# Kernel tuning notes

Measured on AMD Instinct MI355X. Metric: run time of the kernel, lower is better.

Reference implementation:

```python
import jax, jax.numpy as jnp
import numpy as np

B, L, IN_DIM, D_MODEL = 4, 1024, 128, 256
MDIM = 2 * D_MODEL          # mamba_dim = 512 (must equal 2*d_model for shape consistency)
NL = 4                      # mamba_layers
DIN = 2 * MDIM              # d_inner (expand=2)
NST = 16                    # d_state
DTR = MDIM // 16            # dt_rank = 32
KC = 4                      # d_conv
EPS = 1e-5

# sinusoidal positional encoding buffer (deterministic)
_pos = np.arange(L, dtype=np.float32)[:, None]
_div = np.exp(np.arange(0, MDIM, 2, dtype=np.float32) * (-np.log(10000.0) / MDIM))
_pe = np.zeros((L, MDIM), dtype=np.float32)
_pe[:, 0::2] = np.sin(_pos * _div)
_pe[:, 1::2] = np.cos(_pos * _div)
PE = jnp.asarray(_pe)


def setup_inputs() -> dict:
    key = jax.random.key(0)
    ks = iter(jax.random.split(key, 64))
    rn = lambda shape, s=0.02: jax.random.normal(next(ks), shape, jnp.float32) * s
    inp = {
        "x": jax.random.normal(next(ks), (B, L, IN_DIM), jnp.float32),
        "rtg": jax.random.normal(next(ks), (B, L, 1), jnp.float32),
        "state_emb_w": rn((D_MODEL, IN_DIM)), "state_emb_b": jnp.zeros((D_MODEL,)),
        "reward_emb_w": rn((D_MODEL, 1)), "reward_emb_b": jnp.zeros((D_MODEL,)),
        "ln_w": jnp.ones((MDIM,)), "ln_b": jnp.zeros((MDIM,)),
        "in_proj_w": rn((NL, 2 * DIN, MDIM)),
        "conv_w": rn((NL, DIN, KC), 0.1), "conv_b": jnp.zeros((NL, DIN)),
        "x_proj_w": rn((NL, DTR + 2 * NST, DIN)),
        "dt_proj_w": rn((NL, DIN, DTR), 0.1), "dt_proj_b": jnp.full((NL, DIN), -2.0),
        "A_log": jnp.tile(jnp.log(jnp.arange(1, NST + 1, dtype=jnp.float32)), (NL, DIN, 1)),
        "D_param": jnp.ones((NL, DIN)),
        "out_proj_w": rn((NL, MDIM, DIN)),
        "norm_w": jnp.ones((NL, MDIM)), "norm_f_w": jnp.ones((MDIM,)),
        "so_w1": rn((MDIM // 2, MDIM)), "so_b1": jnp.zeros((MDIM // 2,)),
        "so_w2": rn((IN_DIM, MDIM // 2)), "so_b2": jnp.zeros((IN_DIM,)),
        "ro_w1": rn((MDIM // 2, MDIM)), "ro_b1": jnp.zeros((MDIM // 2,)),
        "ro_w2": rn((1, MDIM // 2)), "ro_b2": jnp.zeros((1,)),
    }
    return inp


def _rmsnorm(h, w):
    return h * jax.lax.rsqrt(jnp.mean(h * h, -1, keepdims=True) + EPS) * w


def _mamba(h, ipw, cw, cb, xpw, dpw, dpb, Alog, Dp, opw):
    # h: [B,L,MDIM]
    Ls = h.shape[1]
    xz = h @ ipw.T                                   # [B,L,2*DIN]
    xx, z = jnp.split(xz, 2, axis=-1)
    # causal depthwise conv, kernel KC, left pad KC-1
    xp = jnp.pad(xx, ((0, 0), (KC - 1, 0), (0, 0)))
    xc = cb + sum(cw[:, k] * xp[:, k:k + Ls, :] for k in range(KC))
    xc = jax.nn.silu(xc)                             # [B,L,DIN]
    dbc = xc @ xpw.T                                 # [B,L,DTR+2*NST]
    dt = jax.nn.softplus(dbc[..., :DTR] @ dpw.T + dpb)   # [B,L,DIN]
    Bm = dbc[..., DTR:DTR + NST]                     # [B,L,NST]
    Cm = dbc[..., DTR + NST:]                        # [B,L,NST]
    A = -jnp.exp(Alog)                               # [DIN,NST]

    def step(hc, inp):
        dt_t, B_t, C_t, x_t = inp                    # [B,DIN],[B,NST],[B,NST],[B,DIN]
        hc = jnp.exp(dt_t[:, :, None] * A) * hc + (dt_t * x_t)[:, :, None] * B_t[:, None, :]
        return hc, jnp.einsum('bdn,bn->bd', hc, C_t)

    h0 = jnp.zeros((h.shape[0], DIN, NST), h.dtype)
    _, ys = jax.lax.scan(step, h0, (dt.swapaxes(0, 1), Bm.swapaxes(0, 1),
                                    Cm.swapaxes(0, 1), xc.swapaxes(0, 1)))
    y = ys.swapaxes(0, 1) + Dp * xc
    y = y * jax.nn.silu(z)
    return y @ opw.T                                 # [B,L,MDIM]


def _forward(x, rtg, state_emb_w, state_emb_b, reward_emb_w, reward_emb_b, ln_w, ln_b,
             in_proj_w, conv_w, conv_b, x_proj_w, dt_proj_w, dt_proj_b, A_log, D_param,
             out_proj_w, norm_w, norm_f_w, so_w1, so_b1, so_w2, so_b2, ro_w1, ro_b1, ro_w2, ro_b2):
    se = x @ state_emb_w.T + state_emb_b            # [B,L,D_MODEL]
    re = rtg @ reward_emb_w.T + reward_emb_b        # [B,L,D_MODEL]
    h = jnp.concatenate([se, re], axis=-1)          # [B,L,MDIM]
    h = h + PE[:h.shape[1]]                          # dropout is identity at eval
    mu = jnp.mean(h, -1, keepdims=True)
    var = jnp.var(h, -1, keepdims=True)
    h = (h - mu) * jax.lax.rsqrt(var + EPS) * ln_w + ln_b
    residual = None
    for i in range(NL):
        residual = h if residual is None else h + residual
        hn = _rmsnorm(residual, norm_w[i])
        h = _mamba(hn, in_proj_w[i], conv_w[i], conv_b[i], x_proj_w[i],
                   dt_proj_w[i], dt_proj_b[i], A_log[i], D_param[i], out_proj_w[i])
    residual = h + residual
    h = _rmsnorm(residual, norm_f_w)
    next_state = jax.nn.relu(h @ so_w1.T + so_b1) @ so_w2.T + so_b2   # [B,L,IN_DIM]
    next_reward = jax.nn.relu(h @ ro_w1.T + ro_b1) @ ro_w2.T + ro_b2  # [B,L,1]
    return next_state, next_reward


def reference(x, rtg, state_emb_w, state_emb_b, reward_emb_w, reward_emb_b, ln_w, ln_b,
              in_proj_w, conv_w, conv_b, x_proj_w, dt_proj_w, dt_proj_b, A_log, D_param,
              out_proj_w, norm_w, norm_f_w, so_w1, so_b1, so_w2, so_b2, ro_w1, ro_b1, ro_w2, ro_b2):
    return _forward(x, rtg, state_emb_w, state_emb_b, reward_emb_w, reward_emb_b, ln_w, ln_b,
                    in_proj_w, conv_w, conv_b, x_proj_w, dt_proj_w, dt_proj_b, A_log, D_param,
                    out_proj_w, norm_w, norm_f_w, so_w1, so_b1, so_w2, so_b2, ro_w1, ro_b1, ro_w2, ro_b2)
```

## Files before the change

kernel.cpp:

```cpp
#include <hip/hip_runtime.h>
#include <stdint.h>

typedef unsigned short u16;
typedef __attribute__((ext_vector_type(8))) short bf16x8;
typedef __attribute__((ext_vector_type(8))) u16 u16x8;
typedef __attribute__((ext_vector_type(4))) float f32x4;

static __device__ __forceinline__ u16 f2b(float f) {
  uint32_t u = __builtin_bit_cast(uint32_t, f);
  u += 0x7fffu + ((u >> 16) & 1u);
  return (u16)(u >> 16);
}
static __device__ __forceinline__ float b2f(u16 h) {
  uint32_t u = ((uint32_t)h) << 16;
  return __builtin_bit_cast(float, u);
}

#define GLDS16(gsrc, ldst)                                                        \
  __builtin_amdgcn_global_load_lds(                                               \
      (const __attribute__((address_space(1))) void*)(gsrc),                      \
      (__attribute__((address_space(3))) void*)(ldst), 16, 0, 0)

__global__ __launch_bounds__(256) void setup_kernel(
    const float* __restrict__ ipw, u16* __restrict__ ipwb,
    const float* __restrict__ xpw, u16* __restrict__ xpwb,
    const float* __restrict__ opw, u16* __restrict__ opwb,
    const float* __restrict__ sow1, u16* __restrict__ sow1b,
    const float* __restrict__ sow2, u16* __restrict__ sow2b,
    const float* __restrict__ row1, u16* __restrict__ row1b,
    float* __restrict__ PEt,
    const float* __restrict__ dpw, float* __restrict__ dpwT,
    const float* __restrict__ cw, float* __restrict__ cwT,
    const float* __restrict__ Alog, float* __restrict__ A2T) {
  int i = blockIdx.x * 256 + threadIdx.x;
  if (i < 4194304) { ipwb[i] = f2b(ipw[i]); return; } i -= 4194304;
  if (i < 262144)  { xpwb[i] = f2b(xpw[i]); return; } i -= 262144;
  if (i < 2097152) { opwb[i] = f2b(opw[i]); return; } i -= 2097152;
  if (i < 131072)  { sow1b[i] = f2b(sow1[i]); return; } i -= 131072;
  if (i < 32768)   { sow2b[i] = f2b(sow2[i]); return; } i -= 32768;
  if (i < 131072)  { row1b[i] = f2b(row1[i]); return; } i -= 131072;
  if (i < 524288) {
    int dd = i & 511, l = i >> 9;
    const float cc = -9.210340371976184f / 512.f;
    float div = expf((float)(2 * (dd >> 1)) * cc);
    PEt[i] = (dd & 1) ? cosf((float)l * div) : sinf((float)l * div);
    return;
  } i -= 524288;
  if (i < 131072) {
    int l = i >> 15, r = i & 32767, j = r >> 10, dd = r & 1023;
    dpwT[i] = dpw[(size_t)l * 32768 + (size_t)dd * 32 + j];
    return;
  } i -= 131072;
  if (i < 16384) {
    int l = i >> 12, r = i & 4095, k = r >> 10, dd = r & 1023;
    cwT[i] = cw[(size_t)l * 4096 + (size_t)dd * 4 + k];
    return;
  } i -= 16384;
  if (i < 65536) {
    int l = i >> 14, r = i & 16383, n = r >> 10, d = r & 1023;
    A2T[i] = -expf(Alog[(size_t)l * 16384 + (size_t)d * 16 + n]) * 1.4426950408889634f;
  }
}

__global__ __launch_bounds__(256) void embed_ln2(
    const float* __restrict__ x, const float* __restrict__ rtg,
    const float* __restrict__ Wse, const float* __restrict__ bse,
    const float* __restrict__ Wre, const float* __restrict__ bre,
    const float* __restrict__ lnw, const float* __restrict__ lnb,
    const float* __restrict__ PEt, float* __restrict__ h) {
  const int tid = threadIdx.x;
  const int tok0 = blockIdx.x * 16;
  const int l0 = tok0 & 1023;
  __shared__ float xs[16][128];
  __shared__ float rt[16];
  __shared__ float sw[16][2][4];
  for (int i = tid; i < 16 * 128; i += 256) ((float*)xs)[i] = x[(size_t)tok0 * 128 + i];
  if (tid < 16) rt[tid] = rtg[tok0 + tid];
  __syncthreads();
  const int d = tid;
  float acc[16];
#pragma unroll
  for (int tt = 0; tt < 16; ++tt) acc[tt] = 0.f;
  const float* wrow = Wse + (size_t)d * 128;
  for (int k0 = 0; k0 < 128; k0 += 8) {
    float4 wa = *(const float4*)(wrow + k0);
    float4 wb = *(const float4*)(wrow + k0 + 4);
#pragma unroll
    for (int tt = 0; tt < 16; ++tt) {
      const float* xr = &xs[tt][k0];
      acc[tt] += xr[0] * wa.x + xr[1] * wa.y + xr[2] * wa.z + xr[3] * wa.w +
                 xr[4] * wb.x + xr[5] * wb.y + xr[6] * wb.z + xr[7] * wb.w;
    }
  }
  const float seb = bse[d], reW = Wre[d], reB = bre[d];
  const int lane = tid & 63, wv = tid >> 6;
  float h1a[16];
#pragma unroll
  for (int tt = 0; tt < 16; ++tt) {
    float h0 = acc[tt] + seb + PEt[(size_t)(l0 + tt) * 512 + d];
    float h1 = reB + rt[tt] * reW + PEt[(size_t)(l0 + tt) * 512 + 256 + d];
    acc[tt] = h0;
    h1a[tt] = h1;
    float s = h0 + h1, q = h0 * h0 + h1 * h1;
#pragma unroll
    for (int o = 32; o; o >>= 1) { s += __shfl_xor(s, o); q += __shfl_xor(q, o); }
    if (lane == 0) { sw[tt][0][wv] = s; sw[tt][1][wv] = q; }
  }
  __syncthreads();
#pragma unroll
  for (int tt = 0; tt < 16; ++tt) {
    float S = sw[tt][0][0] + sw[tt][0][1] + sw[tt][0][2] + sw[tt][0][3];
    float Q = sw[tt][1][0] + sw[tt][1][1] + sw[tt][1][2] + sw[tt][1][3];
    float mean = S * (1.f / 512.f);
    float var = Q * (1.f / 512.f) - mean * mean;
    float rstd = rsqrtf(var + 1e-5f);
    size_t base = (size_t)(tok0 + tt) * 512;
    h[base + d]       = (acc[tt] - mean) * rstd * lnw[d] + lnb[d];
    h[base + 256 + d] = (h1a[tt] - mean) * rstd * lnw[256 + d] + lnb[256 + d];
  }
}

__global__ __launch_bounds__(256) void resid_rms_kernel(
    const float* __restrict__ hin, float* __restrict__ residual,
    const float* __restrict__ w, u16* __restrict__ outb, int first) {
  const int tok = blockIdx.x;
  const int t = threadIdx.x;
  __shared__ float rq[4];
  size_t base = (size_t)tok * 512;
  float v0 = hin[base + t], v1 = hin[base + t + 256];
  if (!first) { v0 += residual[base + t]; v1 += residual[base + t + 256]; }
  residual[base + t] = v0;
  residual[base + t + 256] = v1;
  float q = v0 * v0 + v1 * v1;
#pragma unroll
  for (int o = 32; o; o >>= 1) q += __shfl_xor(q, o);
  if ((t & 63) == 0) rq[t >> 6] = q;
  __syncthreads();
  float Q = rq[0] + rq[1] + rq[2] + rq[3];
  float scale = rsqrtf(Q * (1.f / 512.f) + 1e-5f);
  outb[base + t]       = f2b(v0 * scale * w[t]);
  outb[base + t + 256] = f2b(v1 * scale * w[t + 256]);
}

template <int BM, int BN, int WM, int WN, int EPI>
__global__ __launch_bounds__(256) void gemm_bt(
    const u16* __restrict__ A, const u16* __restrict__ Bw,
    float* __restrict__ Cf, u16* __restrict__ Cb,
    const float* __restrict__ bias, const float* __restrict__ bias2,
    int M, int N, int K, int As) {
  constexpr int MF = BM / (WM * 16);
  constexpr int NF = BN / (WN * 16);
  constexpr int NCA = (BM * 4) / 256;
  constexpr int NCB = (BN * 4) / 256;
  __shared__ __align__(16) u16 lA[BM * 32];
  __shared__ __align__(16) u16 lB[BN * 32];
  const int tid = threadIdx.x;
  const int lane = tid & 63;
  const int wv = tid >> 6;
  const int wr = wv / WN, wc = wv % WN;
  const int m0 = blockIdx.x * BM, n0 = blockIdx.y * BN;
  const int kchunk = K / gridDim.z;
  const int kb = blockIdx.z * kchunk;

  f32x4 acc[MF][NF];
#pragma unroll
  for (int i = 0; i < MF; ++i)
#pragma unroll
    for (int j = 0; j < NF; ++j) acc[i][j] = (f32x4){0.f, 0.f, 0.f, 0.f};

  const int srow = tid >> 2, sck = tid & 3;
  const u16* Ag = A + (size_t)(m0 + srow) * As + sck * 8 + kb;
  const u16* Bg = Bw + (size_t)(n0 + srow) * K + sck * 8 + kb;

  for (int k0 = 0; k0 < kchunk; k0 += 32) {
#pragma unroll
    for (int it = 0; it < NCA; ++it)
      GLDS16(Ag + (size_t)it * 64 * As + k0, &lA[(it * 256 + tid) * 8]);
#pragma unroll
    for (int it = 0; it < NCB; ++it)
      GLDS16(Bg + (size_t)it * 64 * K + k0, &lB[(it * 256 + tid) * 8]);
    __syncthreads();
    bf16x8 af[MF], bfr[NF];
    const int koff = (lane >> 4) * 8;
#pragma unroll
    for (int mi = 0; mi < MF; ++mi) {
      int r = wr * (MF * 16) + mi * 16 + (lane & 15);
      af[mi] = *(const bf16x8*)(&lA[r * 32 + koff]);
    }
#pragma unroll
    for (int ni = 0; ni < NF; ++ni) {
      int r = wc * (NF * 16) + ni * 16 + (lane & 15);
      bfr[ni] = *(const bf16x8*)(&lB[r * 32 + koff]);
    }
#pragma unroll
    for (int mi = 0; mi < MF; ++mi)
#pragma unroll
      for (int ni = 0; ni < NF; ++ni)
        acc[mi][ni] = __builtin_amdgcn_mfma_f32_16x16x32_bf16(af[mi], bfr[ni], acc[mi][ni], 0, 0, 0);
    __syncthreads();
  }

  float* co = Cf + (size_t)blockIdx.z * (size_t)M * N;
  const int rbase = (lane >> 4) * 4;
  const int cbase = lane & 15;
#pragma unroll
  for (int mi = 0; mi < MF; ++mi) {
#pragma unroll
    for (int ni = 0; ni < NF; ++ni) {
      int row = m0 + wr * (MF * 16) + mi * 16 + rbase;
      int col = n0 + wc * (NF * 16) + ni * 16 + cbase;
      float bv = 0.f;
      if (EPI == 2 || EPI == 3) bv = bias[col];
      if (EPI == 4) bv = (col < 256) ? bias[col] : bias2[col - 256];
#pragma unroll
      for (int r = 0; r < 4; ++r) {
        float v = acc[mi][ni][r] + bv;
        if (EPI == 2 || EPI == 4) v = fmaxf(v, 0.f);
        size_t idx = (size_t)(row + r) * N + col;
        if (EPI == 1 || EPI == 2 || EPI == 4) Cb[idx] = f2b(v);
        else co[idx] = v;
      }
    }
  }
}

__global__ __launch_bounds__(256) void conv_silu3(
    const u16* __restrict__ xz, const float* __restrict__ cwT,
    const float* __restrict__ cb, u16* __restrict__ xcb) {
  int gid = blockIdx.x * 256 + threadIdx.x;
  int d0 = (gid & 127) * 8;
  int token = gid >> 7;
  int t = token & 1023;
  const u16* xx = xz + (size_t)(token - t) * 2048 + d0;
  float s[8];
  {
    float4 cba = *(const float4*)(cb + d0);
    float4 cbb = *(const float4*)(cb + d0 + 4);
    s[0] = cba.x; s[1] = cba.y; s[2] = cba.z; s[3] = cba.w;
    s[4] = cbb.x; s[5] = cbb.y; s[6] = cbb.z; s[7] = cbb.w;
  }
#pragma unroll
  for (int k = 0; k < 4; ++k) {
    int tt = t - 3 + k;
    if (tt >= 0) {
      u16x8 v = *(const u16x8*)(xx + (size_t)tt * 2048);
      float4 wA = *(const float4*)(cwT + (size_t)k * 1024 + d0);
      float4 wB = *(const float4*)(cwT + (size_t)k * 1024 + d0 + 4);
      s[0] += wA.x * b2f(v[0]); s[1] += wA.y * b2f(v[1]);
      s[2] += wA.z * b2f(v[2]); s[3] += wA.w * b2f(v[3]);
      s[4] += wB.x * b2f(v[4]); s[5] += wB.y * b2f(v[5]);
      s[6] += wB.z * b2f(v[6]); s[7] += wB.w * b2f(v[7]);
    }
  }
  u16x8 o;
#pragma unroll
  for (int j = 0; j < 8; ++j) {
    float sl = s[j] / (1.f + expf(-s[j]));
    o[j] = f2b(sl);
  }
  *(u16x8*)(xcb + (size_t)token * 1024 + d0) = o;
}

__global__ __launch_bounds__(256) void dt_kernel2(
    const float* __restrict__ P, const float* __restrict__ dpwT,
    const float* __restrict__ dpb, u16* __restrict__ dtout,
    float* __restrict__ dbcr) {
  const int tid = threadIdx.x;
  const int tok0 = blockIdx.x * 16;
  __shared__ float sm[16][64];
  const size_t str = (size_t)4096 * 64;
  for (int i = tid; i < 16 * 64; i += 256) {
    size_t o = (size_t)tok0 * 64 + i;
    float v = 0.f;
#pragma unroll
    for (int p = 0; p < 8; ++p) v += P[(size_t)p * str + o];
    ((float*)sm)[i] = v;
    dbcr[o] = v;
  }
  __syncthreads();
  float acc0[16], acc1[16], acc2[16], acc3[16];
#pragma unroll
  for (int t = 0; t < 16; ++t) { acc0[t] = 0.f; acc1[t] = 0.f; acc2[t] = 0.f; acc3[t] = 0.f; }
#pragma unroll 4
  for (int j = 0; j < 32; ++j) {
    float w0 = dpwT[(size_t)j * 1024 + tid];
    float w1 = dpwT[(size_t)j * 1024 + 256 + tid];
    float w2 = dpwT[(size_t)j * 1024 + 512 + tid];
    float w3 = dpwT[(size_t)j * 1024 + 768 + tid];
#pragma unroll
    for (int t = 0; t < 16; ++t) {
      float sv = sm[t][j];
      acc0[t] += sv * w0;
      acc1[t] += sv * w1;
      acc2[t] += sv * w2;
      acc3[t] += sv * w3;
    }
  }
  const float b0 = dpb[tid], b1 = dpb[256 + tid], b2 = dpb[512 + tid], b3 = dpb[768 + tid];
#pragma unroll
  for (int t = 0; t < 16; ++t) {
    size_t o = (size_t)(tok0 + t) * 1024 + tid;
    float a0 = acc0[t] + b0, a1 = acc1[t] + b1, a2 = acc2[t] + b2, a3 = acc3[t] + b3;
    dtout[o]       = f2b((a0 > 20.f) ? a0 : logf(1.f + expf(a0)));
    dtout[o + 256] = f2b((a1 > 20.f) ? a1 : logf(1.f + expf(a1)));
    dtout[o + 512] = f2b((a2 > 20.f) ? a2 : logf(1.f + expf(a2)));
    dtout[o + 768] = f2b((a3 > 20.f) ? a3 : logf(1.f + expf(a3)));
  }
}

__global__ __launch_bounds__(256) void scan1(
    const u16* __restrict__ dt, const u16* __restrict__ xc,
    const float* __restrict__ dbc, const float* __restrict__ A2T_l,
    float* __restrict__ Ubuf, float* __restrict__ SD, int NCc, int TCc) {
  const int d = blockIdx.x * 256 + threadIdx.x;
  const int c = blockIdx.y;
  const int b = blockIdx.z;
  const int t0 = c * TCc;
  __shared__ __align__(16) float sB[64][16];
  for (int i = threadIdx.x; i < TCc * 16; i += 256) {
    int t = i >> 4, n = i & 15;
    sB[t][n] = dbc[((size_t)(b * 1024 + t0 + t)) * 64 + 32 + n];
  }
  float A2[16];
#pragma unroll
  for (int n = 0; n < 16; ++n) A2[n] = A2T_l[(size_t)n * 1024 + d];
  __syncthreads();
  float hc[16];
#pragma unroll
  for (int n = 0; n < 16; ++n) hc[n] = 0.f;
  float sumdt = 0.f;
  size_t tok = (size_t)b * 1024 + t0;
  for (int t = 0; t < TCc; ++t, ++tok) {
    float dtv = b2f(dt[tok * 1024 + d]);
    float xcv = b2f(xc[tok * 1024 + d]);
    float du = dtv * xcv;
    sumdt += dtv;
#pragma unroll
    for (int q = 0; q < 4; ++q) {
      float4 B4 = *(const float4*)(&sB[t][q * 4]);
      float e0 = exp2f(dtv * A2[q * 4 + 0]);
      float e1 = exp2f(dtv * A2[q * 4 + 1]);
      float e2 = exp2f(dtv * A2[q * 4 + 2]);
      float e3 = exp2f(dtv * A2[q * 4 + 3]);
      hc[q * 4 + 0] = e0 * hc[q * 4 + 0] + du * B4.x;
      hc[q * 4 + 1] = e1 * hc[q * 4 + 1] + du * B4.y;
      hc[q * 4 + 2] = e2 * hc[q * 4 + 2] + du * B4.z;
      hc[q * 4 + 3] = e3 * hc[q * 4 + 3] + du * B4.w;
    }
  }
  size_t ob = (((size_t)b * NCc + c) * 16) * 1024 + d;
#pragma unroll
  for (int n = 0; n < 16; ++n) Ubuf[ob + (size_t)n * 1024] = hc[n];
  SD[((size_t)b * NCc + c) * 1024 + d] = sumdt;
}

__global__ __launch_bounds__(256) void scan_mid(
    const float* __restrict__ Ubuf, const float* __restrict__ SD,
    const float* __restrict__ A2T_l, float* __restrict__ H0, int NCc) {
  int idx = blockIdx.x * 256 + threadIdx.x;
  int b = idx >> 14;
  int nd = idx & 16383;
  int d = nd & 1023;
  const float A2 = A2T_l[nd];
  float h = 0.f;
  size_t o0 = ((size_t)b * NCc * 16) * 1024 + nd;
  const size_t cstr = (size_t)16 * 1024;
  size_t sd0 = ((size_t)b * NCc) * 1024 + d;
  for (int cc = 0; cc < NCc; ++cc) {
    size_t o = o0 + (size_t)cc * cstr;
    H0[o] = h;
    if (cc < NCc - 1) {
      float e = exp2f(A2 * SD[sd0 + (size_t)cc * 1024]);
      h = e * h + Ubuf[o];
    }
  }
}

__global__ __launch_bounds__(256) void scan2(
    const u16* __restrict__ dt, const u16* __restrict__ xc,
    const float* __restrict__ dbc, const u16* __restrict__ xz,
    const float* __restrict__ A2T_l, const float* __restrict__ Dp,
    const float* __restrict__ H0, u16* __restrict__ yg, int NCc, int TCc) {
  const int d = blockIdx.x * 256 + threadIdx.x;
  const int c = blockIdx.y;
  const int b = blockIdx.z;
  const int t0 = c * TCc;
  __shared__ __align__(16) float sB[64][16];
  __shared__ __align__(16) float sC[64][16];
  for (int i = threadIdx.x; i < TCc * 16; i += 256) {
    int t = i >> 4, n = i & 15;
    size_t o = ((size_t)(b * 1024 + t0 + t)) * 64 + 32;
    sB[t][n] = dbc[o + n];
    sC[t][n] = dbc[o + 16 + n];
  }
  float A2[16];
#pragma unroll
  for (int n = 0; n < 16; ++n) A2[n] = A2T_l[(size_t)n * 1024 + d];
  const float Dd = Dp[d];
  float hc[16];
  size_t ob = (((size_t)b * NCc + c) * 16) * 1024 + d;
#pragma unroll
  for (int n = 0; n < 16; ++n) hc[n] = H0[ob + (size_t)n * 1024];
  __syncthreads();
  size_t tok = (size_t)b * 1024 + t0;
  for (int t = 0; t < TCc; ++t, ++tok) {
    float dtv = b2f(dt[tok * 1024 + d]);
    float xcv = b2f(xc[tok * 1024 + d]);
    float du = dtv * xcv;
    float y0 = 0.f, y1 = 0.f, y2 = 0.f, y3 = 0.f;
#pragma unroll
    for (int q = 0; q < 4; ++q) {
      float4 B4 = *(const float4*)(&sB[t][q * 4]);
      float4 C4 = *(const float4*)(&sC[t][q * 4]);
      float e0 = exp2f(dtv * A2[q * 4 + 0]);
      float e1 = exp2f(dtv * A2[q * 4 + 1]);
      float e2 = exp2f(dtv * A2[q * 4 + 2]);
      float e3 = exp2f(dtv * A2[q * 4 + 3]);
      hc[q * 4 + 0] = e0 * hc[q * 4 + 0] + du * B4.x;
      hc[q * 4 + 1] = e1 * hc[q * 4 + 1] + du * B4.y;
      hc[q * 4 + 2] = e2 * hc[q * 4 + 2] + du * B4.z;
      hc[q * 4 + 3] = e3 * hc[q * 4 + 3] + du * B4.w;
      y0 += hc[q * 4 + 0] * C4.x;
      y1 += hc[q * 4 + 1] * C4.y;
      y2 += hc[q * 4 + 2] * C4.z;
      y3 += hc[q * 4 + 3] * C4.w;
    }
    float y = (y0 + y1) + (y2 + y3);
    float z = b2f(xz[tok * 2048 + 1024 + d]);
    float g = z / (1.f + expf(-z));
    yg[tok * 1024 + d] = f2b((y + Dd * xcv) * g);
  }
}

__global__ __launch_bounds__(256) void reward_head_kernel(
    const u16* __restrict__ t1sr, const float* __restrict__ w2,
    const float* __restrict__ b2, float* __restrict__ outr) {
  int tok = blockIdx.x * 4 + (threadIdx.x >> 6);
  int lane = threadIdx.x & 63;
  float s = 0.f;
#pragma unroll
  for (int j = 0; j < 256; j += 64)
    s += b2f(t1sr[(size_t)tok * 512 + 256 + j + lane]) * w2[j + lane];
#pragma unroll
  for (int o = 32; o; o >>= 1) s += __shfl_xor(s, o);
  if (lane == 0) outr[tok] = s + b2[0];
}

extern "C" void kernel_launch(void* const* d_in, const int* in_sizes, int n_in,
                              void* d_out, int out_size, void* d_ws, size_t ws_size,
                              hipStream_t stream) {
  const float* x    = (const float*)d_in[0];
  const float* rtg  = (const float*)d_in[1];
  const float* Wse  = (const float*)d_in[2];
  const float* bse  = (const float*)d_in[3];
  const float* Wre  = (const float*)d_in[4];
  const float* bre  = (const float*)d_in[5];
  const float* lnw  = (const float*)d_in[6];
  const float* lnb  = (const float*)d_in[7];
  const float* ipw  = (const float*)d_in[8];
  const float* cw   = (const float*)d_in[9];
  const float* cb   = (const float*)d_in[10];
  const float* xpw  = (const float*)d_in[11];
  const float* dpw  = (const float*)d_in[12];
  const float* dpb  = (const float*)d_in[13];
  const float* Alog = (const float*)d_in[14];
  const float* Dp   = (const float*)d_in[15];
  const float* opw  = (const float*)d_in[16];
  const float* nw   = (const float*)d_in[17];
  const float* nfw  = (const float*)d_in[18];
  const float* sow1 = (const float*)d_in[19];
  const float* sob1 = (const float*)d_in[20];
  const float* sow2 = (const float*)d_in[21];
  const float* sob2 = (const float*)d_in[22];
  const float* row1 = (const float*)d_in[23];
  const float* rob1 = (const float*)d_in[24];
  const float* row2 = (const float*)d_in[25];
  const float* rob2 = (const float*)d_in[26];
  (void)in_sizes; (void)n_in; (void)out_size;

  char* wsp = (char*)d_ws;
  size_t off = 0;
  auto alloc = [&](size_t bytes) -> void* {
    off = (off + 255) & ~(size_t)255;
    void* p = wsp + off;
    off += bytes;
    return p;
  };
  const int TOK = 4096;
  float* h     = (float*)alloc((size_t)TOK * 512 * 4);
  float* resid = (float*)alloc((size_t)TOK * 512 * 4);
  u16* hn      = (u16*)alloc((size_t)TOK * 512 * 2);
  u16* xzb     = (u16*)alloc((size_t)TOK * 2048 * 2);
  u16* xcb     = (u16*)alloc((size_t)TOK * 1024 * 2);
  float* dbcP  = (float*)alloc((size_t)8 * TOK * 64 * 4);
  float* dbc   = (float*)alloc((size_t)TOK * 64 * 4);
  u16* dtb     = (u16*)alloc((size_t)TOK * 1024 * 2);
  float* PEt   = (float*)alloc((size_t)1024 * 512 * 4);
  float* dpwT  = (float*)alloc((size_t)4 * 32 * 1024 * 4);
  float* cwT   = (float*)alloc((size_t)4 * 4 * 1024 * 4);
  float* A2T   = (float*)alloc((size_t)4 * 16 * 1024 * 4);
  u16* ipwb    = (u16*)alloc((size_t)4 * 2048 * 512 * 2);
  u16* xpwb    = (u16*)alloc((size_t)4 * 64 * 1024 * 2);
  u16* opwb    = (u16*)alloc((size_t)4 * 512 * 1024 * 2);
  u16* sow1b   = (u16*)alloc((size_t)256 * 512 * 2);
  u16* row1b   = (u16*)alloc((size_t)256 * 512 * 2);
  u16* sow2b   = (u16*)alloc((size_t)128 * 256 * 2);

  size_t base_off = (off + 255) & ~(size_t)255;
  auto scan_bytes = [](int nc) {
    return (size_t)2 * 4 * nc * 16 * 1024 * 4 + (size_t)4 * nc * 1024 * 4 + 1024;
  };
  int NCc = 16;
  if (ws_size >= base_off + scan_bytes(64)) NCc = 64;
  else if (ws_size >= base_off + scan_bytes(32)) NCc = 32;
  int TCc = 1024 / NCc;
  float* Ubuf  = (float*)alloc((size_t)4096 * NCc * 16 * 4);
  float* H0    = (float*)alloc((size_t)4096 * NCc * 16 * 4);
  float* SD    = (float*)alloc((size_t)4 * NCc * 1024 * 4);
  u16* t1sr    = (u16*)Ubuf;

  setup_kernel<<<29632, 256, 0, stream>>>(ipw, ipwb, xpw, xpwb, opw, opwb,
                                          sow1, sow1b, sow2, sow2b, row1, row1b,
                                          PEt, dpw, dpwT, cw, cwT, Alog, A2T);
  embed_ln2<<<256, 256, 0, stream>>>(x, rtg, Wse, bse, Wre, bre, lnw, lnb, PEt, h);

  for (int i = 0; i < 4; ++i) {
    const float* A2Tl = A2T + (size_t)i * 16 * 1024;
    resid_rms_kernel<<<TOK, 256, 0, stream>>>(h, resid, nw + i * 512, hn, i == 0);
    gemm_bt<128, 128, 2, 2, 1><<<dim3(32, 16, 1), 256, 0, stream>>>(
        hn, ipwb + (size_t)i * 2048 * 512, nullptr, xzb, nullptr, nullptr,
        4096, 2048, 512, 512);
    conv_silu3<<<2048, 256, 0, stream>>>(
        xzb, cwT + (size_t)i * 4096, cb + i * 1024, xcb);
    gemm_bt<64, 64, 2, 2, 0><<<dim3(64, 1, 8), 256, 0, stream>>>(
        xcb, xpwb + (size_t)i * 64 * 1024, dbcP, nullptr, nullptr, nullptr,
        4096, 64, 1024, 1024);
    dt_kernel2<<<TOK / 16, 256, 0, stream>>>(dbcP, dpwT + (size_t)i * 32 * 1024,
                                             dpb + i * 1024, dtb, dbc);
    scan1<<<dim3(4, NCc - 1, 4), 256, 0, stream>>>(
        dtb, xcb, dbc, A2Tl, Ubuf, SD, NCc, TCc);
    scan_mid<<<256, 256, 0, stream>>>(Ubuf, SD, A2Tl, H0, NCc);
    scan2<<<dim3(4, NCc, 4), 256, 0, stream>>>(
        dtb, xcb, dbc, xzb, A2Tl, Dp + i * 1024, H0, xcb, NCc, TCc);
    gemm_bt<64, 64, 2, 2, 0><<<dim3(64, 8, 1), 256, 0, stream>>>(
        xcb, opwb + (size_t)i * 512 * 1024, h, nullptr, nullptr, nullptr,
        4096, 512, 1024, 1024);
  }

  resid_rms_kernel<<<TOK, 256, 0, stream>>>(h, resid, nfw, hn, 0);
  gemm_bt<64, 64, 2, 2, 4><<<dim3(64, 8, 1), 256, 0, stream>>>(
      hn, sow1b, nullptr, t1sr, sob1, rob1, 4096, 512, 512, 512);
  gemm_bt<64, 64, 2, 2, 3><<<dim3(64, 2, 1), 256, 0, stream>>>(
      t1sr, sow2b, (float*)d_out, nullptr, sob2, nullptr, 4096, 128, 256, 512);
  reward_head_kernel<<<TOK / 4, 256, 0, stream>>>(
      t1sr, row2, rob2, (float*)d_out + (size_t)TOK * 128);
}
```

Measured before the change: 646.6 us.

## Fold chunk-state prefix scan into scan2 and drop scan_mid kernel

Removes the separate scan_mid pass that propagated chunk-boundary states into an H0 buffer; each scan2 block now rebuilds its initial state by sequentially combining all preceding chunk summaries from Ubuf and SD. This eliminates one kernel launch per layer and the H0 buffer traffic. In exchange, the prefix work is redundant across chunks, growing quadratically with chunk count and adding exp2f work and load imbalance toward later chunks.

```diff
diff --git a/kernel.cpp b/kernel.cpp
--- a/kernel.cpp
+++ b/kernel.cpp
@@ -354,33 +354,12 @@
   SD[((size_t)b * NCc + c) * 1024 + d] = sumdt;
 }
 
-__global__ __launch_bounds__(256) void scan_mid(
-    const float* __restrict__ Ubuf, const float* __restrict__ SD,
-    const float* __restrict__ A2T_l, float* __restrict__ H0, int NCc) {
-  int idx = blockIdx.x * 256 + threadIdx.x;
-  int b = idx >> 14;
-  int nd = idx & 16383;
-  int d = nd & 1023;
-  const float A2 = A2T_l[nd];
-  float h = 0.f;
-  size_t o0 = ((size_t)b * NCc * 16) * 1024 + nd;
-  const size_t cstr = (size_t)16 * 1024;
-  size_t sd0 = ((size_t)b * NCc) * 1024 + d;
-  for (int cc = 0; cc < NCc; ++cc) {
-    size_t o = o0 + (size_t)cc * cstr;
-    H0[o] = h;
-    if (cc < NCc - 1) {
-      float e = exp2f(A2 * SD[sd0 + (size_t)cc * 1024]);
-      h = e * h + Ubuf[o];
-    }
-  }
-}
-
 __global__ __launch_bounds__(256) void scan2(
     const u16* __restrict__ dt, const u16* __restrict__ xc,
     const float* __restrict__ dbc, const u16* __restrict__ xz,
     const float* __restrict__ A2T_l, const float* __restrict__ Dp,
-    const float* __restrict__ H0, u16* __restrict__ yg, int NCc, int TCc) {
+    const float* __restrict__ Ubuf, const float* __restrict__ SD,
+    u16* __restrict__ yg, int NCc, int TCc) {
   const int d = blockIdx.x * 256 + threadIdx.x;
   const int c = blockIdx.y;
   const int b = blockIdx.z;
@@ -398,9 +377,15 @@
   for (int n = 0; n < 16; ++n) A2[n] = A2T_l[(size_t)n * 1024 + d];
   const float Dd = Dp[d];
   float hc[16];
-  size_t ob = (((size_t)b * NCc + c) * 16) * 1024 + d;
-#pragma unroll
-  for (int n = 0; n < 16; ++n) hc[n] = H0[ob + (size_t)n * 1024];
+#pragma unroll
+  for (int n = 0; n < 16; ++n) hc[n] = 0.f;
+  for (int cc = 0; cc < c; ++cc) {
+    float sd = SD[((size_t)b * NCc + cc) * 1024 + d];
+    size_t oo = (((size_t)b * NCc + cc) * 16) * 1024 + d;
+#pragma unroll
+    for (int n = 0; n < 16; ++n)
+      hc[n] = exp2f(A2[n] * sd) * hc[n] + Ubuf[oo + (size_t)n * 1024];
+  }
   __syncthreads();
   size_t tok = (size_t)b * 1024 + t0;
   for (int t = 0; t < TCc; ++t, ++tok) {
@@ -508,14 +493,13 @@
 
   size_t base_off = (off + 255) & ~(size_t)255;
   auto scan_bytes = [](int nc) {
-    return (size_t)2 * 4 * nc * 16 * 1024 * 4 + (size_t)4 * nc * 1024 * 4 + 1024;
+    return (size_t)4 * nc * 16 * 1024 * 4 + (size_t)4 * nc * 1024 * 4 + 1024;
   };
   int NCc = 16;
   if (ws_size >= base_off + scan_bytes(64)) NCc = 64;
   else if (ws_size >= base_off + scan_bytes(32)) NCc = 32;
   int TCc = 1024 / NCc;
   float* Ubuf  = (float*)alloc((size_t)4096 * NCc * 16 * 4);
-  float* H0    = (float*)alloc((size_t)4096 * NCc * 16 * 4);
   float* SD    = (float*)alloc((size_t)4 * NCc * 1024 * 4);
   u16* t1sr    = (u16*)Ubuf;
 
@@ -539,9 +523,8 @@
                                              dpb + i * 1024, dtb, dbc);
     scan1<<<dim3(4, NCc - 1, 4), 256, 0, stream>>>(
         dtb, xcb, dbc, A2Tl, Ubuf, SD, NCc, TCc);
-    scan_mid<<<256, 256, 0, stream>>>(Ubuf, SD, A2Tl, H0, NCc);
     scan2<<<dim3(4, NCc, 4), 256, 0, stream>>>(
-        dtb, xcb, dbc, xzb, A2Tl, Dp + i * 1024, H0, xcb, NCc, TCc);
+        dtb, xcb, dbc, xzb, A2Tl, Dp + i * 1024, Ubuf, SD, xcb, NCc, TCc);
     gemm_bt<64, 64, 2, 2, 0><<<dim3(64, 8, 1), 256, 0, stream>>>(
         xcb, opwb + (size_t)i * 512 * 1024, h, nullptr, nullptr, nullptr,
         4096, 512, 1024, 1024);
```

Result: slower. 824.9 us (+27.6%).
